# Kernel tuning notes

Hardware: AMD Instinct MI355X
Metric: run time of the kernel (lower is better)

## Reference

```python
import jax, jax.numpy as jnp
import numpy as np

L1, L2, N, C = 4096, 4096, 8, 3


def setup_inputs() -> dict:
    key = jax.random.key(0)
    k1, k2 = jax.random.split(key)
    coords1 = jax.random.uniform(k1, (L1, N, C), dtype=jnp.float32)
    coords2 = jax.random.uniform(k2, (L2, N, C), dtype=jnp.float32)
    return {"coords1": coords1, "coords2": coords2}


def reference(coords1, coords2):
    # coords1: [L1, N, C], coords2: [L2, N, C]
    l1, n, c = coords1.shape
    l2 = coords2.shape[0]
    # Batch-first layout, matching flatten_batch semantics (per-batch NN only)
    q = jnp.swapaxes(coords2, 0, 1)  # [N, L2, C] query points
    r = jnp.swapaxes(coords1, 0, 1)  # [N, L1, C] reference points
    # Squared euclidean distances per batch: [N, L2, L1]
    d2 = (
        jnp.sum(q * q, axis=-1)[:, :, None]
        + jnp.sum(r * r, axis=-1)[:, None, :]
        - 2.0 * jnp.einsum("nlc,nmc->nlm", q, r)
    )
    # tc.nearest returns global flat index; original does fmod(L1) to get the
    # per-batch index — argmin within each batch gives that directly.
    nearest = jnp.argmin(d2, axis=-1)  # [N, L2]
    clusters = nearest.T  # [L2, N]
    # torch.meshgrid(arange(L2), arange(N)) with 'ij' indexing; indices[-1] is
    # the batch index broadcast to [L2, N].
    batch_idx = jnp.broadcast_to(jnp.arange(n, dtype=jnp.int64 if False else jnp.int32), (l2, n))
    return (clusters.reshape(-1), batch_idx.reshape(-1))
```

## Files before the change

kernel.cpp:

```cpp
#include <hip/hip_runtime.h>
#include <float.h>


typedef float v2f __attribute__((ext_vector_type(2)));

constexpr int kL1 = 4096, kL2 = 4096, kN = 8;
constexpr int kChunk = 1024;
constexpr int kQPerBlock = 16;
constexpr int kQ = 4;

__global__ __launch_bounds__(256, 8)
void nearest_kernel(const float* __restrict__ c1, const float* __restrict__ c2,
                    int* __restrict__ out) {
#pragma clang fp contract(off)
  __shared__ float4 refs[kChunk];

  const int tid = threadIdx.x;
  const int n = blockIdx.y;
  const int wave = tid >> 6;
  const int lane = tid & 63;
  const int q0 = blockIdx.x * kQPerBlock + wave * kQ;

  float qx[kQ], qy[kQ], qz[kQ], qqv[kQ];
#pragma unroll
  for (int i = 0; i < kQ; ++i) {
    const float* p = c2 + ((q0 + i) * kN + n) * 3;
    qx[i] = p[0]; qy[i] = p[1]; qz[i] = p[2];
    qqv[i] = __fadd_rn(__fadd_rn(__fmul_rn(qx[i], qx[i]), __fmul_rn(qy[i], qy[i])),
                       __fmul_rn(qz[i], qz[i]));
  }
  const v2f qx01 = {qx[0], qx[1]}, qx23 = {qx[2], qx[3]};
  const v2f qy01 = {qy[0], qy[1]}, qy23 = {qy[2], qy[3]};
  const v2f qz01 = {qz[0], qz[1]}, qz23 = {qz[2], qz[3]};
  const v2f qq01 = {qqv[0], qqv[1]}, qq23 = {qqv[2], qqv[3]};

  float bd[kQ];
  int bi[kQ];
#pragma unroll
  for (int i = 0; i < kQ; ++i) { bd[i] = FLT_MAX; bi[i] = 0; }

  int jcur = lane;

  for (int chunk = 0; chunk < kL1 / kChunk; ++chunk) {
    __syncthreads();

#pragma unroll
    for (int k = 0; k < kChunk / 256; ++k) {
      const int j = tid + 256 * k;
      const float* p = c1 + ((chunk * kChunk + j) * kN + n) * 3;
      const float r0 = p[0], r1 = p[1], r2 = p[2];
      const float rr = __fadd_rn(
          __fadd_rn(__fmul_rn(r0, r0), __fmul_rn(r1, r1)), __fmul_rn(r2, r2));
      refs[j] = make_float4(r0, r1, r2, rr);
    }
    __syncthreads();

#pragma unroll 2
    for (int t = 0; t < kChunk / 64; ++t) {
      const float4 r = refs[t * 64 + lane];
      const v2f rx = {r.x, r.x};
      const v2f ry = {r.y, r.y};
      const v2f rz = {r.z, r.z};
      const v2f rw = {r.w, r.w};

      {
        const v2f m0 = qx01 * rx;
        const v2f m1 = qy01 * ry;
        const v2f s01 = m0 + m1;
        const v2f m2 = qz01 * rz;
        const v2f dot = s01 + m2;
        const v2f A = qq01 + rw;
        const v2f d = __builtin_elementwise_fma((v2f){-2.0f, -2.0f}, dot, A);
        if (d.x < bd[0]) { bd[0] = d.x; bi[0] = jcur; }
        if (d.y < bd[1]) { bd[1] = d.y; bi[1] = jcur; }
      }
      {
        const v2f m0 = qx23 * rx;
        const v2f m1 = qy23 * ry;
        const v2f s01 = m0 + m1;
        const v2f m2 = qz23 * rz;
        const v2f dot = s01 + m2;
        const v2f A = qq23 + rw;
        const v2f d = __builtin_elementwise_fma((v2f){-2.0f, -2.0f}, dot, A);
        if (d.x < bd[2]) { bd[2] = d.x; bi[2] = jcur; }
        if (d.y < bd[3]) { bd[3] = d.y; bi[3] = jcur; }
      }
      jcur += 64;
    }
  }

#pragma unroll
  for (int m = 1; m <= 32; m <<= 1) {
#pragma unroll
    for (int i = 0; i < kQ; ++i) {
      const float od = __shfl_xor(bd[i], m);
      const int oj = __shfl_xor(bi[i], m);
      if (od < bd[i] || (od == bd[i] && oj < bi[i])) { bd[i] = od; bi[i] = oj; }
    }
  }

  if (lane == 0) {
#pragma unroll
    for (int i = 0; i < kQ; ++i) {
      out[(q0 + i) * kN + n] = bi[i];
      out[kL2 * kN + (q0 + i) * kN + n] = n;
    }
  }
}

extern "C" void kernel_launch(void* const* d_in, const int* in_sizes, int n_in,
                              void* d_out, int out_size, void* d_ws, size_t ws_size,
                              hipStream_t stream) {
  const float* c1 = (const float*)d_in[0];
  const float* c2 = (const float*)d_in[1];
  int* out = (int*)d_out;
  dim3 grid(kL2 / kQPerBlock, kN);
  nearest_kernel<<<grid, dim3(256), 0, stream>>>(c1, c2, out);
}
```

Measured before the change: 90.18 us.

## Group four refs per slot, track min slot only, and recover index afterward

Reference points are stored so that each lane handles four consecutive refs per step. The kernel keeps only a per-slot fminf minimum and the slot index, and recomputes the four candidate distances at the end to recover the exact argmin index. Distance math is written as hand-packed v_pk inline asm using op_sel to broadcast ref components, which removes the per-ref compare/select chains and register broadcasts. Launch bounds drop to 4 waves per SIMD to allow more registers. This changes tie-breaking order within groups and relies on bitwise-identical recomputation to match the stored minimum.

```diff
diff --git a/kernel.cpp b/kernel.cpp
--- a/kernel.cpp
+++ b/kernel.cpp
@@ -9,11 +9,26 @@
 constexpr int kQPerBlock = 16;
 constexpr int kQ = 4;
 
-__global__ __launch_bounds__(256, 8)
+__device__ __forceinline__ v2f dist_pk(v2f qx, v2f qy, v2f qz, v2f qq,
+                                       v2f r01, v2f r23, v2f n2) {
+  v2f d, t;
+  asm("v_pk_mul_f32 %0, %2, %6 op_sel:[0,0] op_sel_hi:[1,0]\n\t"
+      "v_pk_mul_f32 %1, %3, %6 op_sel:[0,1] op_sel_hi:[1,1]\n\t"
+      "v_pk_add_f32 %0, %0, %1\n\t"
+      "v_pk_mul_f32 %1, %4, %7 op_sel:[0,0] op_sel_hi:[1,0]\n\t"
+      "v_pk_add_f32 %0, %0, %1\n\t"
+      "v_pk_add_f32 %1, %5, %7 op_sel:[0,1] op_sel_hi:[1,1]\n\t"
+      "v_pk_fma_f32 %0, %0, %8, %1"
+      : "=&v"(d), "=&v"(t)
+      : "v"(qx), "v"(qy), "v"(qz), "v"(qq), "v"(r01), "v"(r23), "v"(n2));
+  return d;
+}
+
+__global__ __launch_bounds__(256, 4)
 void nearest_kernel(const float* __restrict__ c1, const float* __restrict__ c2,
                     int* __restrict__ out) {
 #pragma clang fp contract(off)
-  __shared__ float4 refs[kChunk];
+  __shared__ float4 refs[4][256];
 
   const int tid = threadIdx.x;
   const int n = blockIdx.y;
@@ -21,88 +36,102 @@
   const int lane = tid & 63;
   const int q0 = blockIdx.x * kQPerBlock + wave * kQ;
 
-  float qx[kQ], qy[kQ], qz[kQ], qqv[kQ];
+  float qxs[kQ], qys[kQ], qzs[kQ], qqs[kQ];
 #pragma unroll
   for (int i = 0; i < kQ; ++i) {
     const float* p = c2 + ((q0 + i) * kN + n) * 3;
-    qx[i] = p[0]; qy[i] = p[1]; qz[i] = p[2];
-    qqv[i] = __fadd_rn(__fadd_rn(__fmul_rn(qx[i], qx[i]), __fmul_rn(qy[i], qy[i])),
-                       __fmul_rn(qz[i], qz[i]));
+    qxs[i] = p[0]; qys[i] = p[1]; qzs[i] = p[2];
+    qqs[i] = __fadd_rn(__fadd_rn(__fmul_rn(qxs[i], qxs[i]), __fmul_rn(qys[i], qys[i])),
+                       __fmul_rn(qzs[i], qzs[i]));
   }
-  const v2f qx01 = {qx[0], qx[1]}, qx23 = {qx[2], qx[3]};
-  const v2f qy01 = {qy[0], qy[1]}, qy23 = {qy[2], qy[3]};
-  const v2f qz01 = {qz[0], qz[1]}, qz23 = {qz[2], qz[3]};
-  const v2f qq01 = {qqv[0], qqv[1]}, qq23 = {qqv[2], qqv[3]};
+  const v2f qx01 = {qxs[0], qxs[1]}, qx23 = {qxs[2], qxs[3]};
+  const v2f qy01 = {qys[0], qys[1]}, qy23 = {qys[2], qys[3]};
+  const v2f qz01 = {qzs[0], qzs[1]}, qz23 = {qzs[2], qzs[3]};
+  const v2f qq01 = {qqs[0], qqs[1]}, qq23 = {qqs[2], qqs[3]};
+  const v2f n2 = {-2.0f, -2.0f};
 
-  float bd[kQ];
-  int bi[kQ];
+  float bd[kQ]; int bt[kQ];
 #pragma unroll
-  for (int i = 0; i < kQ; ++i) { bd[i] = FLT_MAX; bi[i] = 0; }
+  for (int i = 0; i < kQ; ++i) { bd[i] = FLT_MAX; bt[i] = 0; }
 
-  int jcur = lane;
-
+  int tg = 0;
   for (int chunk = 0; chunk < kL1 / kChunk; ++chunk) {
     __syncthreads();
 
+    {
+      const int jb = chunk * kChunk + tid * 4;
 #pragma unroll
-    for (int k = 0; k < kChunk / 256; ++k) {
-      const int j = tid + 256 * k;
-      const float* p = c1 + ((chunk * kChunk + j) * kN + n) * 3;
-      const float r0 = p[0], r1 = p[1], r2 = p[2];
-      const float rr = __fadd_rn(
-          __fadd_rn(__fmul_rn(r0, r0), __fmul_rn(r1, r1)), __fmul_rn(r2, r2));
-      refs[j] = make_float4(r0, r1, r2, rr);
+      for (int k = 0; k < 4; ++k) {
+        const float3 rp = *reinterpret_cast<const float3*>(c1 + ((jb + k) * kN + n) * 3);
+        const float rr = __fadd_rn(
+            __fadd_rn(__fmul_rn(rp.x, rp.x), __fmul_rn(rp.y, rp.y)),
+            __fmul_rn(rp.z, rp.z));
+        refs[k][tid] = make_float4(rp.x, rp.y, rp.z, rr);
+      }
     }
     __syncthreads();
 
-#pragma unroll 2
-    for (int t = 0; t < kChunk / 64; ++t) {
-      const float4 r = refs[t * 64 + lane];
-      const v2f rx = {r.x, r.x};
-      const v2f ry = {r.y, r.y};
-      const v2f rz = {r.z, r.z};
-      const v2f rw = {r.w, r.w};
+#pragma unroll
+    for (int t = 0; t < kChunk / 256; ++t, ++tg) {
+      const float4 rA = refs[0][t * 64 + lane];
+      const float4 rB = refs[1][t * 64 + lane];
+      const float4 rC = refs[2][t * 64 + lane];
+      const float4 rD = refs[3][t * 64 + lane];
 
-      {
-        const v2f m0 = qx01 * rx;
-        const v2f m1 = qy01 * ry;
-        const v2f s01 = m0 + m1;
-        const v2f m2 = qz01 * rz;
-        const v2f dot = s01 + m2;
-        const v2f A = qq01 + rw;
-        const v2f d = __builtin_elementwise_fma((v2f){-2.0f, -2.0f}, dot, A);
-        if (d.x < bd[0]) { bd[0] = d.x; bi[0] = jcur; }
-        if (d.y < bd[1]) { bd[1] = d.y; bi[1] = jcur; }
-      }
-      {
-        const v2f m0 = qx23 * rx;
-        const v2f m1 = qy23 * ry;
-        const v2f s01 = m0 + m1;
-        const v2f m2 = qz23 * rz;
-        const v2f dot = s01 + m2;
-        const v2f A = qq23 + rw;
-        const v2f d = __builtin_elementwise_fma((v2f){-2.0f, -2.0f}, dot, A);
-        if (d.x < bd[2]) { bd[2] = d.x; bi[2] = jcur; }
-        if (d.y < bd[3]) { bd[3] = d.y; bi[3] = jcur; }
-      }
-      jcur += 64;
+      const v2f dA01 = dist_pk(qx01, qy01, qz01, qq01, (v2f){rA.x, rA.y}, (v2f){rA.z, rA.w}, n2);
+      const v2f dA23 = dist_pk(qx23, qy23, qz23, qq23, (v2f){rA.x, rA.y}, (v2f){rA.z, rA.w}, n2);
+      const v2f dB01 = dist_pk(qx01, qy01, qz01, qq01, (v2f){rB.x, rB.y}, (v2f){rB.z, rB.w}, n2);
+      const v2f dB23 = dist_pk(qx23, qy23, qz23, qq23, (v2f){rB.x, rB.y}, (v2f){rB.z, rB.w}, n2);
+      const v2f dC01 = dist_pk(qx01, qy01, qz01, qq01, (v2f){rC.x, rC.y}, (v2f){rC.z, rC.w}, n2);
+      const v2f dC23 = dist_pk(qx23, qy23, qz23, qq23, (v2f){rC.x, rC.y}, (v2f){rC.z, rC.w}, n2);
+      const v2f dD01 = dist_pk(qx01, qy01, qz01, qq01, (v2f){rD.x, rD.y}, (v2f){rD.z, rD.w}, n2);
+      const v2f dD23 = dist_pk(qx23, qy23, qz23, qq23, (v2f){rD.x, rD.y}, (v2f){rD.z, rD.w}, n2);
+
+      const float m0 = fminf(fminf(dA01.x, dB01.x), fminf(dC01.x, dD01.x));
+      const float m1 = fminf(fminf(dA01.y, dB01.y), fminf(dC01.y, dD01.y));
+      const float m2 = fminf(fminf(dA23.x, dB23.x), fminf(dC23.x, dD23.x));
+      const float m3 = fminf(fminf(dA23.y, dB23.y), fminf(dC23.y, dD23.y));
+      if (m0 < bd[0]) { bd[0] = m0; bt[0] = tg; }
+      if (m1 < bd[1]) { bd[1] = m1; bt[1] = tg; }
+      if (m2 < bd[2]) { bd[2] = m2; bt[2] = tg; }
+      if (m3 < bd[3]) { bd[3] = m3; bt[3] = tg; }
     }
   }
 
+  int sel[kQ];
+#pragma unroll
+  for (int i = 0; i < kQ; ++i) sel[i] = bt[i] * 64 + lane;
 #pragma unroll
   for (int m = 1; m <= 32; m <<= 1) {
 #pragma unroll
     for (int i = 0; i < kQ; ++i) {
       const float od = __shfl_xor(bd[i], m);
-      const int oj = __shfl_xor(bi[i], m);
-      if (od < bd[i] || (od == bd[i] && oj < bi[i])) { bd[i] = od; bi[i] = oj; }
+      const int os = __shfl_xor(sel[i], m);
+      if (od < bd[i] || (od == bd[i] && os < sel[i])) { bd[i] = od; sel[i] = os; }
     }
   }
 
-  if (lane == 0) {
 #pragma unroll
-    for (int i = 0; i < kQ; ++i) {
-      out[(q0 + i) * kN + n] = bi[i];
+  for (int i = 0; i < kQ; ++i) {
+    if (lane == i) {
+      const int j0 = sel[i] * 4;
+      float dc[4];
+#pragma unroll
+      for (int k = 0; k < 4; ++k) {
+        const float3 rp = *reinterpret_cast<const float3*>(c1 + ((j0 + k) * kN + n) * 3);
+        const float rr = __fadd_rn(
+            __fadd_rn(__fmul_rn(rp.x, rp.x), __fmul_rn(rp.y, rp.y)),
+            __fmul_rn(rp.z, rp.z));
+        const float dot = __fadd_rn(
+            __fadd_rn(__fmul_rn(qxs[i], rp.x), __fmul_rn(qys[i], rp.y)),
+            __fmul_rn(qzs[i], rp.z));
+        dc[k] = __fmaf_rn(-2.0f, dot, __fadd_rn(qqs[i], rr));
+      }
+      int kk = 3;
+      if (dc[2] == bd[i]) kk = 2;
+      if (dc[1] == bd[i]) kk = 1;
+      if (dc[0] == bd[i]) kk = 0;
+      out[(q0 + i) * kN + n] = j0 + kk;
       out[kL2 * kN + (q0 + i) * kN + n] = n;
     }
   }
```

Result: slower. 99.19 us (+10.0%).
